# Optimization experiments

Hardware: AMD Instinct MI355X
Metric: run time of the kernel (lower is better)

The kernel has to match this reference:

```python
import jax, jax.numpy as jnp
import numpy as np

N, B, E, H, L, NF = 32768, 2048, 524288, 128, 7, 10
NODE_F = 60  # 10 frames * (loc 3 + vel 3)
OUT_F = 30   # 10 frames * 3


def _mlp(x, W1, b1, W2, b2):
    return jax.nn.relu(x @ W1 + b1) @ W2 + b2


def _lin(key, fan_in, fan_out):
    s = 1.0 / np.sqrt(fan_in)
    kw, kb = jax.random.split(key)
    W = jax.random.uniform(kw, (fan_in, fan_out), jnp.float32, -s, s)
    b = jax.random.uniform(kb, (fan_out,), jnp.float32, -s, s)
    return W, b


def setup_inputs() -> dict:
    key = jax.random.key(0)
    ks = jax.random.split(key, 12)
    p = {}
    p["loc"] = jax.random.normal(ks[0], (N, NF, 3), jnp.float32)
    p["vel"] = jax.random.normal(ks[1], (N, NF, 3), jnp.float32)
    p["y"] = jax.random.normal(ks[2], (N, NF, 3), jnp.float32)
    p["edge_index"] = jax.random.randint(ks[3], (2, E), 0, N, dtype=jnp.int64)
    p["batch_size"] = B
    # embedder: Linear(60,H) -> ReLU -> Linear(H,H)
    p["emb_W1"], p["emb_b1"] = _lin(ks[4], NODE_F, H)
    p["emb_W2"], p["emb_b2"] = _lin(ks[5], H, H)
    # per-layer message net Linear(2H,H)->ReLU->Linear(H,H); update net Linear(2H,H)->ReLU->Linear(H,H)
    mW1, mb1, mW2, mb2, uW1, ub1, uW2, ub2 = [], [], [], [], [], [], [], []
    for i in range(L):
        k = jax.random.fold_in(ks[6], i)
        k1, k2, k3, k4 = jax.random.split(k, 4)
        a, b = _lin(k1, 2 * H, H); mW1.append(a); mb1.append(b)
        a, b = _lin(k2, H, H); mW2.append(a); mb2.append(b)
        a, b = _lin(k3, 2 * H, H); uW1.append(a); ub1.append(b)
        a, b = _lin(k4, H, H); uW2.append(a); ub2.append(b)
    p["msg_W1"] = jnp.stack(mW1); p["msg_b1"] = jnp.stack(mb1)
    p["msg_W2"] = jnp.stack(mW2); p["msg_b2"] = jnp.stack(mb2)
    p["upd_W1"] = jnp.stack(uW1); p["upd_b1"] = jnp.stack(ub1)
    p["upd_W2"] = jnp.stack(uW2); p["upd_b2"] = jnp.stack(ub2)
    # head: Linear(H,H) -> ReLU -> Linear(H,30)
    p["head_W1"], p["head_b1"] = _lin(ks[7], H, H)
    p["head_W2"], p["head_b2"] = _lin(ks[8], H, OUT_F)
    return p


def reference(loc, vel, y, edge_index, batch_size,
              emb_W1, emb_b1, emb_W2, emb_b2,
              msg_W1, msg_b1, msg_W2, msg_b2,
              upd_W1, upd_b1, upd_W2, upd_b2,
              head_W1, head_b1, head_W2, head_b2):
    n = loc.shape[0]
    src, dst = edge_index[0], edge_index[1]  # x_j = x[src], x_i = x[dst] (PyG source_to_target)
    x = jnp.concatenate([loc, vel], axis=-1).reshape(n, -1)  # (N, 60)
    x = _mlp(x, emb_W1, emb_b1, emb_W2, emb_b2)              # (N, H)
    for i in range(L):
        m_in = jnp.concatenate([x[dst], x[src]], axis=-1)    # (E, 2H) cat(x_i, x_j)
        msg = _mlp(m_in, msg_W1[i], msg_b1[i], msg_W2[i], msg_b2[i])  # (E, H)
        agg = jax.ops.segment_sum(msg, dst, num_segments=n)  # scatter-add at targets
        x = _mlp(jnp.concatenate([x, agg], axis=-1), upd_W1[i], upd_b1[i], upd_W2[i], upd_b2[i])
    x = _mlp(x, head_W1, head_b1, head_W2, head_b2)          # (N, 30)
    loc_pred = x.reshape(n, NF, 3) + loc
    d = jnp.sqrt(jnp.sum((loc_pred - y) ** 2, axis=-1))      # (N, NF)
    ade_loss = d.reshape(batch_size, -1, NF).mean(axis=-1).mean(axis=-1)  # (B,)
    fde = jnp.sqrt(jnp.sum((loc_pred[:, -1, :] - y[:, -1, :]) ** 2, axis=-1))  # (N,)
    fde_loss = fde.reshape(batch_size, -1).mean(axis=-1)     # (B,)
    backprop_loss = ade_loss.mean()
    return backprop_loss, ade_loss, fde_loss
```

## Files before the change

### kernel.cpp

```cpp
#include <hip/hip_runtime.h>
#include <hip/hip_bf16.h>
#include <stdint.h>

#define HH 128

typedef __attribute__((ext_vector_type(8))) short short8;
typedef __attribute__((ext_vector_type(4))) float floatx4;

typedef __attribute__((address_space(3))) uint32_t lds_u32_t;
typedef const __attribute__((address_space(1))) uint32_t gbl_u32_t;

__device__ __forceinline__ void gl_lds16(const void* g, void* l) {
  __builtin_amdgcn_global_load_lds((gbl_u32_t*)g, (lds_u32_t*)l, 16, 0, 0);
}

__device__ __forceinline__ float bf2f(short v) {
  union { uint32_t u; float f; } x; x.u = ((uint32_t)(uint16_t)v) << 16; return x.f;
}
__device__ __forceinline__ short f2bf(float f) {
  union { float f; uint32_t u; } x; x.f = f;
  uint32_t r = x.u + 0x7fffu + ((x.u >> 16) & 1u);
  return (short)(r >> 16);
}
__device__ __forceinline__ float rdf(const void* p, int i, int fl) {
  return fl ? bf2f(((const short*)p)[i]) : ((const float*)p)[i];
}


__global__ void detect_zero(const int* __restrict__ eidx, int* iflag, int* dflag,
                            int* __restrict__ counts, float* accp, int* ticket,
                            const uint32_t* __restrict__ loc, int N) {
  int g = blockIdx.x * 256 + threadIdx.x;
  if (g < N) counts[g] = 0;
  if (blockIdx.x == 0) {
    __shared__ int nz, cnt;
    if (threadIdx.x == 0) { nz = 0; cnt = 0; *accp = 0.f; *ticket = 0; }
    __syncthreads();
    int any = 0;
    for (int i = threadIdx.x; i < 1024; i += 256) any |= (eidx[2 * i + 1] != 0);
    if (any) atomicOr(&nz, 1);
    uint32_t u = loc[threadIdx.x];
    int e = (u >> 7) & 0xFF;
    if (e >= 100 && e <= 140) atomicAdd(&cnt, 1);
    __syncthreads();
    if (threadIdx.x == 0) {
      *iflag = (nz == 0) ? 1 : 0;
      *dflag = (cnt >= 192) ? 1 : 0;
    }
  }
}


__global__ void pad_input(const void* __restrict__ loc, const void* __restrict__ vel,
                          short* __restrict__ dst, const int* __restrict__ dflag) {
  int fl = *dflag;
  int idx = blockIdx.x * 256 + threadIdx.x;
  int j = idx & 63, i = idx >> 6;
  short v = 0;
  if (j < 60) {
    int f = j / 6, c = j % 6;
    float x = (c < 3) ? rdf(loc, (i * 10 + f) * 3 + c, fl)
                      : rdf(vel, (i * 10 + f) * 3 + (c - 3), fl);
    v = f2bf(x);
  }
  dst[idx] = v;
}

struct WPrep {
  const void* src[8];
  unsigned long long dstoff[8];
  int L[8], K[8], Nn[8], Kp[8], Np[8];
  int bstart[9];
};

__global__ void prep_w(WPrep a, short* __restrict__ wbase, const int* __restrict__ dflag) {
  int fl = *dflag;
  int b = blockIdx.x;
  int s = 0;
  while (b >= a.bstart[s + 1]) ++s;
  int idx = (b - a.bstart[s]) * 256 + threadIdx.x;
  int Kp = a.Kp[s], Np = a.Np[s], K = a.K[s], Nn = a.Nn[s];
  int tot = a.L[s] * Np * Kp;
  if (idx >= tot) return;
  int k = idx % Kp; int rest = idx / Kp; int n = rest % Np; int l = rest / Np;
  short v = 0;
  if (k < K && n < Nn) v = f2bf(rdf(a.src[s], (l * K + k) * Nn + n, fl));
  wbase[a.dstoff[s] + idx] = v;
}

struct BPrep {
  const void* src[8];
  int n[8];
  int estart[9];
};

__global__ void prep_b(BPrep a, float* __restrict__ bias, const int* __restrict__ dflag) {
  int fl = *dflag;
  int idx = blockIdx.x * 256 + threadIdx.x;
  if (idx >= a.estart[8]) return;
  int s = 0;
  while (idx >= a.estart[s + 1]) ++s;
  int j = idx - a.estart[s];
  bias[idx] = (j < a.n[s]) ? rdf(a.src[s], j, fl) : 0.0f;
}


__global__ void fold_kernel(const short* __restrict__ msgW1T, const short* __restrict__ msgW2T,
                            const short* __restrict__ updW1T, const short* __restrict__ updW2T,
                            const short* __restrict__ headW1T,
                            const float* __restrict__ msgB1f, const float* __restrict__ msgB2f,
                            const float* __restrict__ updB1f, const float* __restrict__ updB2f,
                            const float* __restrict__ headB1f,
                            short* __restrict__ fmats, float* __restrict__ fbias) {
  if (blockIdx.x < 1664) {
    int idx = blockIdx.x * 256 + threadIdx.x;
    if (idx >= 26 * 16384) return;
    int k = idx & 127; int n = (idx >> 7) & 127; int m = idx >> 14;
    const short* w2;
    const short* rhs;
    if (m < 7) {
      w2 = msgW2T + m * 16384;
      rhs = updW1T + m * 32768 + n * 256 + 128;
    } else if (m < 14) {
      int l = m - 7;
      w2 = updW2T + l * 16384;
      rhs = (l < 6) ? (msgW1T + (l + 1) * 32768 + n * 256) : (headW1T + n * 128);
    } else if (m < 20) {
      int l = m - 14;
      w2 = updW2T + l * 16384;
      rhs = msgW1T + (l + 1) * 32768 + n * 256 + 128;
    } else {
      int l = m - 20;
      w2 = updW2T + l * 16384;
      rhs = updW1T + (l + 1) * 32768 + n * 256;
    }
    float s = 0.f;
    for (int j = 0; j < 128; ++j) s += bf2f(w2[j * 128 + k]) * bf2f(rhs[j]);
    fmats[idx] = f2bf(s);
  } else {
    int idx = (blockIdx.x - 1664) * 256 + threadIdx.x;
    if (idx >= 26 * 128) return;
    int n = idx & 127; int m = idx >> 7;
    float s = 0.f;
    if (m < 7) {
      const short* u1 = updW1T + m * 32768 + n * 256 + 128;
      for (int j = 0; j < 128; ++j) s += msgB2f[m * 128 + j] * bf2f(u1[j]);
    } else if (m < 14) {
      int l = m - 7;
      if (l < 6) {
        const short* m1 = msgW1T + (l + 1) * 32768 + n * 256;
        for (int j = 0; j < 128; ++j) s += updB2f[l * 128 + j] * bf2f(m1[j]);
        s += msgB1f[(l + 1) * 128 + n];
      } else {
        const short* h1 = headW1T + n * 128;
        for (int j = 0; j < 128; ++j) s += updB2f[6 * 128 + j] * bf2f(h1[j]);
        s += headB1f[n];
      }
    } else if (m < 20) {
      int l = m - 14;
      const short* m1 = msgW1T + (l + 1) * 32768 + n * 256 + 128;
      for (int j = 0; j < 128; ++j) s += updB2f[l * 128 + j] * bf2f(m1[j]);
    } else {
      int l = m - 20;
      const short* u1 = updW1T + (l + 1) * 32768 + n * 256;
      for (int j = 0; j < 128; ++j) s += updB2f[l * 128 + j] * bf2f(u1[j]);
      s += updB1f[(l + 1) * 128 + n];
    }
    fbias[m * 128 + n] = s;
  }
}


__global__ void hist_kernel(const int* __restrict__ eidx, const int* __restrict__ iflag,
                            int* __restrict__ counts, int E) {
  int e = blockIdx.x * 256 + threadIdx.x;
  if (e >= E) return;
  int fl = *iflag;
  int d = fl ? eidx[2 * (E + e)] : eidx[E + e];
  atomicAdd(&counts[d], 1);
}

__global__ void scan_bsum(const int* __restrict__ counts, int* __restrict__ bsums, int N) {
  int i = blockIdx.x * 256 + threadIdx.x;
  int v = (i < N) ? counts[i] : 0;
#pragma unroll
  for (int off = 1; off < 64; off <<= 1) v += __shfl_xor(v, off);
  __shared__ int ws4[4];
  if ((threadIdx.x & 63) == 0) ws4[threadIdx.x >> 6] = v;
  __syncthreads();
  if (threadIdx.x == 0) bsums[blockIdx.x] = ws4[0] + ws4[1] + ws4[2] + ws4[3];
}

__global__ void scan_final(const int* __restrict__ counts, const int* __restrict__ bsums,
                           int* __restrict__ row_start, int* __restrict__ cursor,
                           float* __restrict__ deg, int N, int E) {
  int t = threadIdx.x;
  __shared__ int shb[2];
  __shared__ int wsum[4];
  int v = (t < 128 && t < (int)blockIdx.x) ? bsums[t] : 0;
#pragma unroll
  for (int off = 1; off < 64; off <<= 1) v += __shfl_xor(v, off);
  if (t == 0) shb[0] = v;
  if (t == 64) shb[1] = v;
  int i = blockIdx.x * 256 + t;
  int c = (i < N) ? counts[i] : 0;
  int lane = t & 63, w = t >> 6;
  int x = c;
#pragma unroll
  for (int off = 1; off < 64; off <<= 1) {
    int u = __shfl_up(x, off);
    if (lane >= off) x += u;
  }
  if (lane == 63) wsum[w] = x;
  __syncthreads();
  int wpre = 0;
#pragma unroll
  for (int k = 0; k < 4; ++k)
    if (k < w) wpre += wsum[k];
  int excl = shb[0] + shb[1] + wpre + x - c;
  if (i < N) {
    row_start[i] = excl;
    cursor[i] = excl;
    deg[i] = (float)c;
  }
  if (i == N - 1) row_start[N] = E;
}

__global__ void scatter_kernel(const int* __restrict__ eidx, const int* __restrict__ iflag,
                               int* __restrict__ cursor, int* __restrict__ ssrc, int E) {
  int e = blockIdx.x * 256 + threadIdx.x;
  if (e >= E) return;
  int fl = *iflag;
  int d = fl ? eidx[2 * (E + e)] : eidx[E + e];
  int sv = fl ? eidx[2 * e] : eidx[e];
  int pos = atomicAdd(&cursor[d], 1);
  ssrc[pos] = sv;
}


__global__ __launch_bounds__(256)
void edge_agg(const uint32_t* __restrict__ Pp, const uint32_t* __restrict__ Qp,
              const int* __restrict__ ssrc, const int* __restrict__ row_start,
              uint32_t* __restrict__ Hagg, int Ntot) {
  int w = threadIdx.x >> 6, lane = threadIdx.x & 63;
  int d = blockIdx.x * 4 + w;
  if (d >= Ntot) return;
  uint32_t pv = Pp[(size_t)d * 64 + lane];
  float px = bf2f((short)(pv & 0xffff));
  float py = bf2f((short)(pv >> 16));
  int s0 = row_start[d], s1 = row_start[d + 1];
  float ax = 0.f, ay = 0.f;
  int e = s0;
  for (; e + 8 <= s1; e += 8) {
    int idx[8]; uint32_t q[8];
#pragma unroll
    for (int u = 0; u < 8; ++u) idx[u] = ssrc[e + u];
#pragma unroll
    for (int u = 0; u < 8; ++u) q[u] = Qp[(size_t)idx[u] * 64 + lane];
#pragma unroll
    for (int u = 0; u < 8; ++u) {
      float hx = px + bf2f((short)(q[u] & 0xffff));
      float hy = py + bf2f((short)(q[u] >> 16));
      ax += hx > 0.f ? hx : 0.f;
      ay += hy > 0.f ? hy : 0.f;
    }
  }
  if (e + 4 <= s1) {
    int idx[4]; uint32_t q[4];
#pragma unroll
    for (int u = 0; u < 4; ++u) idx[u] = ssrc[e + u];
#pragma unroll
    for (int u = 0; u < 4; ++u) q[u] = Qp[(size_t)idx[u] * 64 + lane];
#pragma unroll
    for (int u = 0; u < 4; ++u) {
      float hx = px + bf2f((short)(q[u] & 0xffff));
      float hy = py + bf2f((short)(q[u] >> 16));
      ax += hx > 0.f ? hx : 0.f;
      ay += hy > 0.f ? hy : 0.f;
    }
    e += 4;
  }
  if (e + 2 <= s1) {
    int i0 = ssrc[e], i1 = ssrc[e + 1];
    uint32_t q0 = Qp[(size_t)i0 * 64 + lane];
    uint32_t q1 = Qp[(size_t)i1 * 64 + lane];
    float hx = px + bf2f((short)(q0 & 0xffff)), hy = py + bf2f((short)(q0 >> 16));
    ax += hx > 0.f ? hx : 0.f; ay += hy > 0.f ? hy : 0.f;
    hx = px + bf2f((short)(q1 & 0xffff)); hy = py + bf2f((short)(q1 >> 16));
    ax += hx > 0.f ? hx : 0.f; ay += hy > 0.f ? hy : 0.f;
    e += 2;
  }
  if (e < s1) {
    int i0 = ssrc[e];
    uint32_t q0 = Qp[(size_t)i0 * 64 + lane];
    float hx = px + bf2f((short)(q0 & 0xffff));
    float hy = py + bf2f((short)(q0 >> 16));
    ax += hx > 0.f ? hx : 0.f;
    ay += hy > 0.f ? hy : 0.f;
  }
  uint32_t packed = (uint32_t)(uint16_t)f2bf(ax) | ((uint32_t)(uint16_t)f2bf(ay) << 16);
  Hagg[(size_t)d * 64 + lane] = packed;
}


__device__ __forceinline__ void write_aslots64(char* lds, const floatx4 v[2][4],
                                               int wr, int wc, int quad, int l16) {
#pragma unroll
  for (int mt = 0; mt < 2; ++mt) {
    int g = wr * 2 + mt;
#pragma unroll
    for (int nt = 0; nt < 4; ++nt) {
      int s2 = wc * 2 + (nt >> 1);
      int qc = (nt & 1) * 2 + (l16 >> 3);
      char* base = lds + (size_t)(s2 * 4 + g) * 1024 + 2 * (l16 & 7);
#pragma unroll
      for (int r = 0; r < 4; ++r)
        *(short*)(base + (quad * 4 + r + 16 * qc) * 16) = f2bf(v[mt][nt][r]);
    }
  }
}

template <int NT, int TS>
__device__ __forceinline__ void gemm64(const char* lds, int wr, int wc,
                                       floatx4 acc[2][NT], int lane) {
  const char* ldsB = lds + 16384;
#pragma unroll
  for (int s2 = 0; s2 < 4; ++s2) {
    short8 af[2];
#pragma unroll
    for (int mt = 0; mt < 2; ++mt)
      af[mt] = *(const short8*)(lds + (s2 * 4 + wr * 2 + mt) * 1024 + lane * 16);
    short8 bf[NT];
#pragma unroll
    for (int nt = 0; nt < NT; ++nt)
      bf[nt] = *(const short8*)(ldsB + (s2 * TS + wc * NT + nt) * 1024 + lane * 16);
#pragma unroll
    for (int mt = 0; mt < 2; ++mt)
#pragma unroll
      for (int nt = 0; nt < NT; ++nt)
        acc[mt][nt] = __builtin_amdgcn_mfma_f32_16x16x32_bf16(af[mt], bf[nt], acc[mt][nt], 0, 0, 0);
  }
}

__device__ __forceinline__ void stage128(const short* M, int stride, char* ldsB,
                                         int w, int lane, int quad, int l16) {
#pragma unroll
  for (int c = 0; c < 8; ++c) {
    int slot = w * 8 + c, s2 = slot >> 3, t = slot & 7;
    gl_lds16(M + (t * 16 + l16) * stride + s2 * 32 + quad * 8,
             ldsB + slot * 1024 + lane * 16);
  }
}


template <int MODE>
__global__ __launch_bounds__(256, 3)
void mlp_fused(const short* __restrict__ Ain, const short* __restrict__ XUin,
               const short* __restrict__ W1s, const float* __restrict__ b1s,
               const short* __restrict__ W2s, const float* __restrict__ b2s,
               const short* __restrict__ W3s, const float* __restrict__ b3s,
               const short* __restrict__ W4s, const float* __restrict__ b4s,
               const float* __restrict__ deg,
               short* __restrict__ Pout, short* __restrict__ Qout,
               short* __restrict__ XUout, float* __restrict__ out32) {
  __shared__ __align__(16) char lds[49152];
  char* ldsB = lds + 16384;

  const int tid = threadIdx.x;
  const int w = tid >> 6, lane = tid & 63;
  const int quad = lane >> 4, l16 = lane & 15;
  const int wr = w >> 1, wc = w & 1;
  const int R0 = blockIdx.x * 64;
  const int CB = wc * 64;

  floatx4 zero4 = {0.f, 0.f, 0.f, 0.f};
  floatx4 acc[2][4];

  if constexpr (MODE == 0) {
#pragma unroll
    for (int c = 0; c < 4; ++c) {
      int slot = w * 4 + c, s = slot >> 3, t = slot & 7;
      gl_lds16(W1s + (t * 16 + l16) * 64 + s * 32 + quad * 8,
               ldsB + slot * 1024 + lane * 16);
    }
    short8 afrag[2][2];
#pragma unroll
    for (int mt = 0; mt < 2; ++mt) {
      int m = R0 + wr * 32 + mt * 16 + l16;
      const short* pr = Ain + (size_t)m * 64;
#pragma unroll
      for (int s = 0; s < 2; ++s) afrag[s][mt] = *(const short8*)(pr + s * 32 + quad * 8);
    }
    float b1f[4], b2f[4], pa[4], pc[4];
#pragma unroll
    for (int t = 0; t < 4; ++t) {
      int col = CB + t * 16 + l16;
      b1f[t] = b1s[col]; b2f[t] = b2s[col]; pa[t] = b3s[col]; pc[t] = b4s[col];
    }
#pragma unroll
    for (int mt = 0; mt < 2; ++mt)
#pragma unroll
      for (int t = 0; t < 4; ++t) acc[mt][t] = zero4;
    __syncthreads();
#pragma unroll
    for (int s = 0; s < 2; ++s) {
      short8 bfrag[4];
#pragma unroll
      for (int nt = 0; nt < 4; ++nt)
        bfrag[nt] = *(const short8*)(ldsB + (s * 8 + wc * 4 + nt) * 1024 + lane * 16);
#pragma unroll
      for (int mt = 0; mt < 2; ++mt)
#pragma unroll
        for (int nt = 0; nt < 4; ++nt)
          acc[mt][nt] = __builtin_amdgcn_mfma_f32_16x16x32_bf16(afrag[s][mt], bfrag[nt], acc[mt][nt], 0, 0, 0);
    }
    __syncthreads();
    stage128(W2s, 128, ldsB, w, lane, quad, l16);
    {
      floatx4 hv[2][4];
#pragma unroll
      for (int mt = 0; mt < 2; ++mt)
#pragma unroll
        for (int nt = 0; nt < 4; ++nt)
#pragma unroll
          for (int r = 0; r < 4; ++r) {
            float h = acc[mt][nt][r] + b1f[nt];
            hv[mt][nt][r] = h > 0.f ? h : 0.f;
          }
      write_aslots64(lds, hv, wr, wc, quad, l16);
    }
    __syncthreads();
    floatx4 accx[2][4];
#pragma unroll
    for (int mt = 0; mt < 2; ++mt)
#pragma unroll
      for (int t = 0; t < 4; ++t) accx[mt][t] = zero4;
    gemm64<4, 8>(lds, wr, wc, accx, lane);
    floatx4 xv[2][4];
#pragma unroll
    for (int mt = 0; mt < 2; ++mt)
#pragma unroll
      for (int nt = 0; nt < 4; ++nt)
#pragma unroll
        for (int r = 0; r < 4; ++r)
          xv[mt][nt][r] = accx[mt][nt][r] + b2f[nt];
    __syncthreads();
    write_aslots64(lds, xv, wr, wc, quad, l16);
    stage128(W3s, 256, ldsB, w, lane, quad, l16);
    __syncthreads();
    floatx4 ap[2][4];
#pragma unroll
    for (int mt = 0; mt < 2; ++mt)
#pragma unroll
      for (int t = 0; t < 4; ++t) ap[mt][t] = zero4;
    gemm64<4, 8>(lds, wr, wc, ap, lane);
#pragma unroll
    for (int mt = 0; mt < 2; ++mt)
#pragma unroll
      for (int nt = 0; nt < 4; ++nt) {
        int col = CB + nt * 16 + l16;
#pragma unroll
        for (int r = 0; r < 4; ++r) {
          int row = R0 + wr * 32 + mt * 16 + quad * 4 + r;
          Pout[(size_t)row * HH + col] = f2bf(ap[mt][nt][r] + pa[nt]);
        }
      }
    __syncthreads();
    stage128(W3s + 128, 256, ldsB, w, lane, quad, l16);
    __syncthreads();
    floatx4 aq[2][4];
#pragma unroll
    for (int mt = 0; mt < 2; ++mt)
#pragma unroll
      for (int t = 0; t < 4; ++t) aq[mt][t] = zero4;
    gemm64<4, 8>(lds, wr, wc, aq, lane);
#pragma unroll
    for (int mt = 0; mt < 2; ++mt)
#pragma unroll
      for (int nt = 0; nt < 4; ++nt) {
        int col = CB + nt * 16 + l16;
#pragma unroll
        for (int r = 0; r < 4; ++r) {
          int row = R0 + wr * 32 + mt * 16 + quad * 4 + r;
          Qout[(size_t)row * HH + col] = f2bf(aq[mt][nt][r]);
        }
      }
    __syncthreads();
    stage128(W4s, 256, ldsB, w, lane, quad, l16);
    __syncthreads();
    floatx4 au[2][4];
#pragma unroll
    for (int mt = 0; mt < 2; ++mt)
#pragma unroll
      for (int t = 0; t < 4; ++t) au[mt][t] = zero4;
    gemm64<4, 8>(lds, wr, wc, au, lane);
#pragma unroll
    for (int mt = 0; mt < 2; ++mt)
#pragma unroll
      for (int nt = 0; nt < 4; ++nt) {
        int col = CB + nt * 16 + l16;
#pragma unroll
        for (int r = 0; r < 4; ++r) {
          int row = R0 + wr * 32 + mt * 16 + quad * 4 + r;
          XUout[(size_t)row * HH + col] = f2bf(au[mt][nt][r] + pc[nt]);
        }
      }
    return;
  } else {
    stage128(W1s, 128, ldsB, w, lane, quad, l16);
    short8 hfrag[4][2];
#pragma unroll
    for (int mt = 0; mt < 2; ++mt) {
      int m = R0 + wr * 32 + mt * 16 + l16;
      const short* pr = Ain + (size_t)m * HH;
#pragma unroll
      for (int s = 0; s < 4; ++s) hfrag[s][mt] = *(const short8*)(pr + s * 32 + quad * 8);
    }
    float b2u[4], pa[4], pb[4], pc[4];
#pragma unroll
    for (int t = 0; t < 4; ++t) {
      int col = CB + t * 16 + l16;
      b2u[t] = b1s[col];
      pa[t] = b2s[col];
      if constexpr (MODE == 2) { pb[t] = b3s[col]; pc[t] = b4s[col]; }
    }
    float dvals[2][4];
#pragma unroll
    for (int mt = 0; mt < 2; ++mt)
#pragma unroll
      for (int r = 0; r < 4; ++r)
        dvals[mt][r] = deg[R0 + wr * 32 + mt * 16 + quad * 4 + r];
#pragma unroll
    for (int mt = 0; mt < 2; ++mt)
#pragma unroll
      for (int nt = 0; nt < 4; ++nt) {
        int col = CB + nt * 16 + l16;
#pragma unroll
        for (int r = 0; r < 4; ++r) {
          int row = R0 + wr * 32 + mt * 16 + quad * 4 + r;
          acc[mt][nt][r] = bf2f(XUin[(size_t)row * HH + col]) + dvals[mt][r] * b2u[nt];
        }
      }
    __syncthreads();
#pragma unroll
    for (int s = 0; s < 4; ++s) {
      short8 bfrag[4];
#pragma unroll
      for (int nt = 0; nt < 4; ++nt)
        bfrag[nt] = *(const short8*)(ldsB + (s * 8 + wc * 4 + nt) * 1024 + lane * 16);
#pragma unroll
      for (int mt = 0; mt < 2; ++mt)
#pragma unroll
        for (int nt = 0; nt < 4; ++nt)
          acc[mt][nt] = __builtin_amdgcn_mfma_f32_16x16x32_bf16(hfrag[s][mt], bfrag[nt], acc[mt][nt], 0, 0, 0);
    }
    __syncthreads();
    stage128(W2s, 128, ldsB, w, lane, quad, l16);
    {
      floatx4 hv[2][4];
#pragma unroll
      for (int mt = 0; mt < 2; ++mt)
#pragma unroll
        for (int nt = 0; nt < 4; ++nt)
#pragma unroll
          for (int r = 0; r < 4; ++r) {
            float h = acc[mt][nt][r];
            hv[mt][nt][r] = h > 0.f ? h : 0.f;
          }
      write_aslots64(lds, hv, wr, wc, quad, l16);
    }
    __syncthreads();
    floatx4 ap[2][4];
#pragma unroll
    for (int mt = 0; mt < 2; ++mt)
#pragma unroll
      for (int t = 0; t < 4; ++t) ap[mt][t] = zero4;
    gemm64<4, 8>(lds, wr, wc, ap, lane);

    if constexpr (MODE == 2) {
#pragma unroll
      for (int mt = 0; mt < 2; ++mt)
#pragma unroll
        for (int nt = 0; nt < 4; ++nt) {
          int col = CB + nt * 16 + l16;
#pragma unroll
          for (int r = 0; r < 4; ++r) {
            int row = R0 + wr * 32 + mt * 16 + quad * 4 + r;
            Pout[(size_t)row * HH + col] = f2bf(ap[mt][nt][r] + pa[nt]);
          }
        }
      __syncthreads();
      stage128(W3s, 128, ldsB, w, lane, quad, l16);
      __syncthreads();
      floatx4 aq[2][4];
#pragma unroll
      for (int mt = 0; mt < 2; ++mt)
#pragma unroll
        for (int t = 0; t < 4; ++t) aq[mt][t] = zero4;
      gemm64<4, 8>(lds, wr, wc, aq, lane);
#pragma unroll
      for (int mt = 0; mt < 2; ++mt)
#pragma unroll
        for (int nt = 0; nt < 4; ++nt) {
          int col = CB + nt * 16 + l16;
#pragma unroll
          for (int r = 0; r < 4; ++r) {
            int row = R0 + wr * 32 + mt * 16 + quad * 4 + r;
            Qout[(size_t)row * HH + col] = f2bf(aq[mt][nt][r] + pb[nt]);
          }
        }
      __syncthreads();
      stage128(W4s, 128, ldsB, w, lane, quad, l16);
      __syncthreads();
      floatx4 au[2][4];
#pragma unroll
      for (int mt = 0; mt < 2; ++mt)
#pragma unroll
        for (int t = 0; t < 4; ++t) au[mt][t] = zero4;
      gemm64<4, 8>(lds, wr, wc, au, lane);
#pragma unroll
      for (int mt = 0; mt < 2; ++mt)
#pragma unroll
        for (int nt = 0; nt < 4; ++nt) {
          int col = CB + nt * 16 + l16;
#pragma unroll
          for (int r = 0; r < 4; ++r) {
            int row = R0 + wr * 32 + mt * 16 + quad * 4 + r;
            XUout[(size_t)row * HH + col] = f2bf(au[mt][nt][r] + pc[nt]);
          }
        }
    } else {
      floatx4 h2[2][4];
#pragma unroll
      for (int mt = 0; mt < 2; ++mt)
#pragma unroll
        for (int nt = 0; nt < 4; ++nt)
#pragma unroll
          for (int r = 0; r < 4; ++r) {
            float h = ap[mt][nt][r] + pa[nt];
            h2[mt][nt][r] = h > 0.f ? h : 0.f;
          }
      __syncthreads();
      write_aslots64(lds, h2, wr, wc, quad, l16);
#pragma unroll
      for (int c = 0; c < 2; ++c) {
        int slot = w * 2 + c, s2 = slot >> 1, t = slot & 1;
        gl_lds16(W3s + (t * 16 + l16) * 128 + s2 * 32 + quad * 8,
                 ldsB + slot * 1024 + lane * 16);
      }
      __syncthreads();
      floatx4 acco[2][1];
#pragma unroll
      for (int mt = 0; mt < 2; ++mt) acco[mt][0] = zero4;
      gemm64<1, 2>(lds, wr, wc, acco, lane);
      float ob = b3s[wc * 16 + l16];
#pragma unroll
      for (int mt = 0; mt < 2; ++mt) {
        int col = wc * 16 + l16;
#pragma unroll
        for (int r = 0; r < 4; ++r) {
          int row = R0 + wr * 32 + mt * 16 + quad * 4 + r;
          out32[(size_t)row * 32 + col] = acco[mt][0][r] + ob;
        }
      }
    }
  }
}


__global__ void loss_kernel(const float* __restrict__ out32, const void* __restrict__ loc,
                            const void* __restrict__ yv, const int* __restrict__ dflag,
                            float* __restrict__ out, float* __restrict__ acc,
                            int* __restrict__ ticket, int NB, int nblocks, float inv) {
  int fl = *dflag;
  int i = blockIdx.x * 256 + threadIdx.x;
  const float* o = out32 + (size_t)i * 32;
  float dsum = 0.f, fde = 0.f;
#pragma unroll
  for (int f = 0; f < 10; ++f) {
    float dx = o[f * 3 + 0] + rdf(loc, i * 30 + f * 3 + 0, fl) - rdf(yv, i * 30 + f * 3 + 0, fl);
    float dy = o[f * 3 + 1] + rdf(loc, i * 30 + f * 3 + 1, fl) - rdf(yv, i * 30 + f * 3 + 1, fl);
    float dz = o[f * 3 + 2] + rdf(loc, i * 30 + f * 3 + 2, fl) - rdf(yv, i * 30 + f * 3 + 2, fl);
    float d = sqrtf(dx * dx + dy * dy + dz * dz);
    dsum += d;
    if (f == 9) fde = d;
  }
#pragma unroll
  for (int m = 1; m < 16; m <<= 1) {
    dsum += __shfl_xor(dsum, m);
    fde += __shfl_xor(fde, m);
  }
  if ((threadIdx.x & 15) == 0) {
    int b = i >> 4;
    out[1 + b] = dsum / 160.0f;
    out[1 + NB + b] = fde / 16.0f;
    unsafeAtomicAdd(acc, dsum);
  }
  __threadfence();
  __syncthreads();
  if (threadIdx.x == 0) {
    int old = atomicAdd(ticket, 1);
    if (old == nblocks - 1) {
      float v = unsafeAtomicAdd(acc, 0.0f);
      out[0] = v * inv;
    }
  }
}


extern "C" void kernel_launch(void* const* d_in, const int* in_sizes, int n_in,
                              void* d_out, int out_size, void* d_ws, size_t ws_size,
                              hipStream_t stream) {
  const void* loc = d_in[0];
  const void* vel = d_in[1];
  const void* yv = d_in[2];
  const int* eidx = (const int*)d_in[3];

  const int N = in_sizes[0] / 30;
  const int E = in_sizes[3] / 2;
  const int L = 7;
  const int NB = N / 16;

  const size_t MB = 1024 * 1024;
  char* ws = (char*)d_ws;
  short* XU = (short*)ws;
  short* P = (short*)(ws + 8 * MB);
  short* Qs = (short*)(ws + 24 * MB);
  short* Hagg = (short*)(ws + 32 * MB);
  short* fmats = (short*)(ws + 40 * MB);
  int* bsums = (int*)(ws + 41 * MB);
  short* wbase = (short*)(ws + 48 * MB);
  const unsigned long long OFF_EMBW1 = 0;
  const unsigned long long OFF_EMBW2 = 8192;
  const unsigned long long OFF_HEADW1 = 24576;
  const unsigned long long OFF_HEADW2 = 40960;
  const unsigned long long OFF_MSGW1 = 45056;
  const unsigned long long OFF_MSGW2 = 274432;
  const unsigned long long OFF_UPDW1 = 389120;
  const unsigned long long OFF_UPDW2 = 618496;
  short* embW1T = wbase + OFF_EMBW1;
  short* embW2T = wbase + OFF_EMBW2;
  short* headW1T = wbase + OFF_HEADW1;
  short* headW2T = wbase + OFF_HEADW2;
  short* msgW1T = wbase + OFF_MSGW1;
  short* msgW2T = wbase + OFF_MSGW2;
  short* updW1T = wbase + OFF_UPDW1;
  short* updW2T = wbase + OFF_UPDW2;
  float* bias = (float*)(ws + 49 * MB + 512 * 1024);
  float* embB1f = bias;
  float* embB2f = bias + 128;
  float* msgB1f = bias + 256;
  float* msgB2f = bias + 1152;
  float* updB1f = bias + 2048;
  float* updB2f = bias + 2944;
  float* headB1f = bias + 3840;
  float* headB2f = bias + 3968;
  float* fbias = (float*)(ws + 49 * MB + 640 * 1024);
  int* counts = (int*)(ws + 49 * MB + 768 * 1024);
  int* row_start = (int*)(ws + 50 * MB);
  int* cursor = (int*)(ws + 50 * MB + 256 * 1024);
  float* deg = (float*)(ws + 50 * MB + 512 * 1024);
  int* iflag = (int*)(ws + 50 * MB + 768 * 1024);
  int* dflag = iflag + 16;
  float* accp = (float*)(iflag + 32);
  int* ticket = iflag + 48;
  int* ssrc = (int*)(ws + 51 * MB);
  short* in64 = (short*)(ws + 53 * MB);
  float* out32 = (float*)(ws + 57 * MB);

  const int NBLK = (N + 255) / 256;

  detect_zero<<<NBLK, 256, 0, stream>>>(eidx, iflag, dflag, counts, accp, ticket,
                                        (const uint32_t*)loc, N);
  hist_kernel<<<(E + 255) / 256, 256, 0, stream>>>(eidx, iflag, counts, E);
  scan_bsum<<<NBLK, 256, 0, stream>>>(counts, bsums, N);
  scan_final<<<NBLK, 256, 0, stream>>>(counts, bsums, row_start, cursor, deg, N, E);
  scatter_kernel<<<(E + 255) / 256, 256, 0, stream>>>(eidx, iflag, cursor, ssrc, E);

  pad_input<<<(N * 64) / 256, 256, 0, stream>>>(loc, vel, in64, dflag);

  {
    WPrep a;
    const void* srcs[8] = {d_in[5], d_in[7], d_in[17], d_in[19],
                           d_in[9], d_in[11], d_in[13], d_in[15]};
    unsigned long long offs[8] = {OFF_EMBW1, OFF_EMBW2, OFF_HEADW1, OFF_HEADW2,
                                  OFF_MSGW1, OFF_MSGW2, OFF_UPDW1, OFF_UPDW2};
    int Ls[8] = {1, 1, 1, 1, 7, 7, 7, 7};
    int Ks[8] = {60, 128, 128, 128, 256, 128, 256, 128};
    int Ns[8] = {128, 128, 128, 30, 128, 128, 128, 128};
    int Kps[8] = {64, 128, 128, 128, 256, 128, 256, 128};
    int Nps[8] = {128, 128, 128, 32, 128, 128, 128, 128};
    int cum = 0;
    for (int s = 0; s < 8; ++s) {
      a.src[s] = srcs[s]; a.dstoff[s] = offs[s];
      a.L[s] = Ls[s]; a.K[s] = Ks[s]; a.Nn[s] = Ns[s]; a.Kp[s] = Kps[s]; a.Np[s] = Nps[s];
      a.bstart[s] = cum;
      cum += (Ls[s] * Nps[s] * Kps[s] + 255) / 256;
    }
    a.bstart[8] = cum;
    prep_w<<<cum, 256, 0, stream>>>(a, wbase, dflag);
  }
  {
    BPrep a;
    const void* srcs[8] = {d_in[6], d_in[8], d_in[10], d_in[12],
                           d_in[14], d_in[16], d_in[18], d_in[20]};
    int ns[8] = {128, 128, 896, 896, 896, 896, 128, 30};
    int es[9] = {0, 128, 256, 1152, 2048, 2944, 3840, 3968, 4000};
    for (int s = 0; s < 8; ++s) { a.src[s] = srcs[s]; a.n[s] = ns[s]; a.estart[s] = es[s]; }
    a.estart[8] = es[8];
    prep_b<<<16, 256, 0, stream>>>(a, bias, dflag);
  }

  fold_kernel<<<1664 + 13, 256, 0, stream>>>(msgW1T, msgW2T, updW1T, updW2T, headW1T,
                                             msgB1f, msgB2f, updB1f, updB2f, headB1f,
                                             fmats, fbias);

  mlp_fused<0><<<N / 64, 256, 0, stream>>>(in64, nullptr,
      embW1T, embB1f, embW2T, embB2f,
      msgW1T, msgB1f, updW1T, updB1f,
      nullptr, P, Qs, XU, nullptr);

  for (int l = 0; l < L; ++l) {
    edge_agg<<<(N + 3) / 4, 256, 0, stream>>>((const uint32_t*)P, (const uint32_t*)Qs,
                                              ssrc, row_start, (uint32_t*)Hagg, N);
    if (l < L - 1) {
      mlp_fused<2><<<N / 64, 256, 0, stream>>>(Hagg, XU,
          fmats + l * 16384, fbias + l * 128,
          fmats + (7 + l) * 16384, fbias + (7 + l) * 128,
          fmats + (14 + l) * 16384, fbias + (14 + l) * 128,
          fmats + (20 + l) * 16384, fbias + (20 + l) * 128,
          deg, P, Qs, XU, nullptr);
    } else {
      mlp_fused<3><<<N / 64, 256, 0, stream>>>(Hagg, XU,
          fmats + 6 * 16384, fbias + 6 * 128,
          fmats + 13 * 16384, fbias + 13 * 128,
          headW2T, headB2f,
          nullptr, nullptr,
          deg, nullptr, nullptr, nullptr, out32);
    }
  }

  loss_kernel<<<N / 256, 256, 0, stream>>>(out32, loc, yv, dflag, (float*)d_out, accp,
                                           ticket, NB, N / 256, 1.0f / 327680.0f);
}
```

Measured before the change: 485.9 us.

## Fuse loss into final MLP, store XU fragment-native, unroll edge gather

The loss computation moves into the last fused MLP kernel: head outputs are staged in LDS and reduced per block, which drops the separate loss kernel and the out32 round trip through global memory. The XU intermediate is now stored in a per-thread fragment-native layout, so writes and reads become contiguous vectorized accesses instead of scattered 16-bit stores. The edge aggregation loop gains a 16-wide unrolled gather to keep more loads in flight, at the cost of higher register pressure. The XU layout change only works because every kernel that touches XU agrees on the new per-thread layout.

```diff
diff --git a/kernel.cpp b/kernel.cpp
--- a/kernel.cpp
+++ b/kernel.cpp
@@ -6,6 +6,7 @@
 
 typedef __attribute__((ext_vector_type(8))) short short8;
 typedef __attribute__((ext_vector_type(4))) float floatx4;
+typedef __attribute__((ext_vector_type(4))) uint32_t uint4v;
 
 typedef __attribute__((address_space(3))) uint32_t lds_u32_t;
 typedef const __attribute__((address_space(1))) uint32_t gbl_u32_t;
@@ -24,6 +25,9 @@
 }
 __device__ __forceinline__ float rdf(const void* p, int i, int fl) {
   return fl ? bf2f(((const short*)p)[i]) : ((const float*)p)[i];
+}
+__device__ __forceinline__ uint32_t packbf(float a, float b) {
+  return (uint32_t)(uint16_t)f2bf(a) | ((uint32_t)(uint16_t)f2bf(b) << 16);
 }
 
 
@@ -251,7 +255,21 @@
   int s0 = row_start[d], s1 = row_start[d + 1];
   float ax = 0.f, ay = 0.f;
   int e = s0;
-  for (; e + 8 <= s1; e += 8) {
+  for (; e + 16 <= s1; e += 16) {
+    int idx[16]; uint32_t q[16];
+#pragma unroll
+    for (int u = 0; u < 16; ++u) idx[u] = ssrc[e + u];
+#pragma unroll
+    for (int u = 0; u < 16; ++u) q[u] = Qp[(size_t)idx[u] * 64 + lane];
+#pragma unroll
+    for (int u = 0; u < 16; ++u) {
+      float hx = px + bf2f((short)(q[u] & 0xffff));
+      float hy = py + bf2f((short)(q[u] >> 16));
+      ax += hx > 0.f ? hx : 0.f;
+      ay += hy > 0.f ? hy : 0.f;
+    }
+  }
+  if (e + 8 <= s1) {
     int idx[8]; uint32_t q[8];
 #pragma unroll
     for (int u = 0; u < 8; ++u) idx[u] = ssrc[e + u];
@@ -264,6 +282,7 @@
       ax += hx > 0.f ? hx : 0.f;
       ay += hy > 0.f ? hy : 0.f;
     }
+    e += 8;
   }
   if (e + 4 <= s1) {
     int idx[4]; uint32_t q[4];
@@ -298,8 +317,7 @@
     ax += hx > 0.f ? hx : 0.f;
     ay += hy > 0.f ? hy : 0.f;
   }
-  uint32_t packed = (uint32_t)(uint16_t)f2bf(ax) | ((uint32_t)(uint16_t)f2bf(ay) << 16);
-  Hagg[(size_t)d * 64 + lane] = packed;
+  Hagg[(size_t)d * 64 + lane] = packbf(ax, ay);
 }
 
 
@@ -362,7 +380,11 @@
                const short* __restrict__ W4s, const float* __restrict__ b4s,
                const float* __restrict__ deg,
                short* __restrict__ Pout, short* __restrict__ Qout,
-               short* __restrict__ XUout, float* __restrict__ out32) {
+               short* __restrict__ XUout,
+               const void* __restrict__ locp, const void* __restrict__ yvp,
+               const int* __restrict__ dflagp, float* __restrict__ lossout,
+               float* __restrict__ accg, int* __restrict__ ticketp,
+               int NBv, int nbl, float inv) {
   __shared__ __align__(16) char lds[49152];
   char* ldsB = lds + 16384;
 
@@ -494,17 +516,16 @@
 #pragma unroll
       for (int t = 0; t < 4; ++t) au[mt][t] = zero4;
     gemm64<4, 8>(lds, wr, wc, au, lane);
-#pragma unroll
-    for (int mt = 0; mt < 2; ++mt)
-#pragma unroll
-      for (int nt = 0; nt < 4; ++nt) {
-        int col = CB + nt * 16 + l16;
-#pragma unroll
-        for (int r = 0; r < 4; ++r) {
-          int row = R0 + wr * 32 + mt * 16 + quad * 4 + r;
-          XUout[(size_t)row * HH + col] = f2bf(au[mt][nt][r] + pc[nt]);
-        }
-      }
+    {
+      uint32_t* xpw = (uint32_t*)XUout + ((size_t)(blockIdx.x * 256) + tid) * 16;
+#pragma unroll
+      for (int mt = 0; mt < 2; ++mt)
+#pragma unroll
+        for (int nt = 0; nt < 4; ++nt) {
+          xpw[(mt * 4 + nt) * 2 + 0] = packbf(au[mt][nt][0] + pc[nt], au[mt][nt][1] + pc[nt]);
+          xpw[(mt * 4 + nt) * 2 + 1] = packbf(au[mt][nt][2] + pc[nt], au[mt][nt][3] + pc[nt]);
+        }
+    }
     return;
   } else {
     stage128(W1s, 128, ldsB, w, lane, quad, l16);
@@ -530,17 +551,27 @@
 #pragma unroll
       for (int r = 0; r < 4; ++r)
         dvals[mt][r] = deg[R0 + wr * 32 + mt * 16 + quad * 4 + r];
-#pragma unroll
-    for (int mt = 0; mt < 2; ++mt)
-#pragma unroll
-      for (int nt = 0; nt < 4; ++nt) {
-        int col = CB + nt * 16 + l16;
-#pragma unroll
-        for (int r = 0; r < 4; ++r) {
-          int row = R0 + wr * 32 + mt * 16 + quad * 4 + r;
-          acc[mt][nt][r] = bf2f(XUin[(size_t)row * HH + col]) + dvals[mt][r] * b2u[nt];
-        }
+    {
+      const uint4v* xp = (const uint4v*)((const uint32_t*)XUin +
+                                         ((size_t)(blockIdx.x * 256) + tid) * 16);
+      uint32_t xw[16];
+#pragma unroll
+      for (int k2 = 0; k2 < 4; ++k2) {
+        uint4v v = xp[k2];
+#pragma unroll
+        for (int j = 0; j < 4; ++j) xw[k2 * 4 + j] = v[j];
       }
+#pragma unroll
+      for (int mt = 0; mt < 2; ++mt)
+#pragma unroll
+        for (int nt = 0; nt < 4; ++nt) {
+          uint32_t u0 = xw[(mt * 4 + nt) * 2], u1 = xw[(mt * 4 + nt) * 2 + 1];
+          acc[mt][nt][0] = bf2f((short)(u0 & 0xffff)) + dvals[mt][0] * b2u[nt];
+          acc[mt][nt][1] = bf2f((short)(u0 >> 16)) + dvals[mt][1] * b2u[nt];
+          acc[mt][nt][2] = bf2f((short)(u1 & 0xffff)) + dvals[mt][2] * b2u[nt];
+          acc[mt][nt][3] = bf2f((short)(u1 >> 16)) + dvals[mt][3] * b2u[nt];
+        }
+    }
     __syncthreads();
 #pragma unroll
     for (int s = 0; s < 4; ++s) {
@@ -618,17 +649,16 @@
 #pragma unroll
         for (int t = 0; t < 4; ++t) au[mt][t] = zero4;
       gemm64<4, 8>(lds, wr, wc, au, lane);
-#pragma unroll
-      for (int mt = 0; mt < 2; ++mt)
-#pragma unroll
-        for (int nt = 0; nt < 4; ++nt) {
-          int col = CB + nt * 16 + l16;
-#pragma unroll
-          for (int r = 0; r < 4; ++r) {
-            int row = R0 + wr * 32 + mt * 16 + quad * 4 + r;
-            XUout[(size_t)row * HH + col] = f2bf(au[mt][nt][r] + pc[nt]);
+      {
+        uint32_t* xpw = (uint32_t*)XUout + ((size_t)(blockIdx.x * 256) + tid) * 16;
+#pragma unroll
+        for (int mt = 0; mt < 2; ++mt)
+#pragma unroll
+          for (int nt = 0; nt < 4; ++nt) {
+            xpw[(mt * 4 + nt) * 2 + 0] = packbf(au[mt][nt][0] + pc[nt], au[mt][nt][1] + pc[nt]);
+            xpw[(mt * 4 + nt) * 2 + 1] = packbf(au[mt][nt][2] + pc[nt], au[mt][nt][3] + pc[nt]);
           }
-        }
+      }
     } else {
       floatx4 h2[2][4];
 #pragma unroll
@@ -654,55 +684,53 @@
       for (int mt = 0; mt < 2; ++mt) acco[mt][0] = zero4;
       gemm64<1, 2>(lds, wr, wc, acco, lane);
       float ob = b3s[wc * 16 + l16];
+      __syncthreads();
+      float* lot = (float*)lds;
 #pragma unroll
       for (int mt = 0; mt < 2; ++mt) {
-        int col = wc * 16 + l16;
+        int colL = wc * 16 + l16;
 #pragma unroll
         for (int r = 0; r < 4; ++r) {
-          int row = R0 + wr * 32 + mt * 16 + quad * 4 + r;
-          out32[(size_t)row * 32 + col] = acco[mt][0][r] + ob;
+          int rowL = wr * 32 + mt * 16 + quad * 4 + r;
+          lot[rowL * 32 + colL] = acco[mt][0][r] + ob;
         }
       }
-    }
-  }
-}
-
-
-__global__ void loss_kernel(const float* __restrict__ out32, const void* __restrict__ loc,
-                            const void* __restrict__ yv, const int* __restrict__ dflag,
-                            float* __restrict__ out, float* __restrict__ acc,
-                            int* __restrict__ ticket, int NB, int nblocks, float inv) {
-  int fl = *dflag;
-  int i = blockIdx.x * 256 + threadIdx.x;
-  const float* o = out32 + (size_t)i * 32;
-  float dsum = 0.f, fde = 0.f;
-#pragma unroll
-  for (int f = 0; f < 10; ++f) {
-    float dx = o[f * 3 + 0] + rdf(loc, i * 30 + f * 3 + 0, fl) - rdf(yv, i * 30 + f * 3 + 0, fl);
-    float dy = o[f * 3 + 1] + rdf(loc, i * 30 + f * 3 + 1, fl) - rdf(yv, i * 30 + f * 3 + 1, fl);
-    float dz = o[f * 3 + 2] + rdf(loc, i * 30 + f * 3 + 2, fl) - rdf(yv, i * 30 + f * 3 + 2, fl);
-    float d = sqrtf(dx * dx + dy * dy + dz * dz);
-    dsum += d;
-    if (f == 9) fde = d;
-  }
-#pragma unroll
-  for (int m = 1; m < 16; m <<= 1) {
-    dsum += __shfl_xor(dsum, m);
-    fde += __shfl_xor(fde, m);
-  }
-  if ((threadIdx.x & 15) == 0) {
-    int b = i >> 4;
-    out[1 + b] = dsum / 160.0f;
-    out[1 + NB + b] = fde / 16.0f;
-    unsafeAtomicAdd(acc, dsum);
-  }
-  __threadfence();
-  __syncthreads();
-  if (threadIdx.x == 0) {
-    int old = atomicAdd(ticket, 1);
-    if (old == nblocks - 1) {
-      float v = unsafeAtomicAdd(acc, 0.0f);
-      out[0] = v * inv;
+      __syncthreads();
+      int fl = *dflagp;
+      if (tid < 64) {
+        int node = R0 + tid;
+        const float* o = lot + tid * 32;
+        float dsum = 0.f, fde = 0.f;
+#pragma unroll
+        for (int f = 0; f < 10; ++f) {
+          float dx = o[f * 3 + 0] + rdf(locp, node * 30 + f * 3 + 0, fl) - rdf(yvp, node * 30 + f * 3 + 0, fl);
+          float dy = o[f * 3 + 1] + rdf(locp, node * 30 + f * 3 + 1, fl) - rdf(yvp, node * 30 + f * 3 + 1, fl);
+          float dz = o[f * 3 + 2] + rdf(locp, node * 30 + f * 3 + 2, fl) - rdf(yvp, node * 30 + f * 3 + 2, fl);
+          float d = sqrtf(dx * dx + dy * dy + dz * dz);
+          dsum += d;
+          if (f == 9) fde = d;
+        }
+#pragma unroll
+        for (int m = 1; m < 16; m <<= 1) {
+          dsum += __shfl_xor(dsum, m);
+          fde += __shfl_xor(fde, m);
+        }
+        if ((tid & 15) == 0) {
+          int b = node >> 4;
+          lossout[1 + b] = dsum / 160.0f;
+          lossout[1 + NBv + b] = fde / 16.0f;
+          unsafeAtomicAdd(accg, dsum);
+        }
+      }
+      __threadfence();
+      __syncthreads();
+      if (tid == 0) {
+        int old = atomicAdd(ticketp, 1);
+        if (old == nbl - 1) {
+          float v = unsafeAtomicAdd(accg, 0.0f);
+          lossout[0] = v * inv;
+        }
+      }
     }
   }
 }
@@ -766,7 +794,6 @@
   int* ticket = iflag + 48;
   int* ssrc = (int*)(ws + 51 * MB);
   short* in64 = (short*)(ws + 53 * MB);
-  float* out32 = (float*)(ws + 57 * MB);
 
   const int NBLK = (N + 255) / 256;
 
@@ -818,7 +845,8 @@
   mlp_fused<0><<<N / 64, 256, 0, stream>>>(in64, nullptr,
       embW1T, embB1f, embW2T, embB2f,
       msgW1T, msgB1f, updW1T, updB1f,
-      nullptr, P, Qs, XU, nullptr);
+      nullptr, P, Qs, XU,
+      nullptr, nullptr, nullptr, nullptr, nullptr, nullptr, 0, 0, 0.0f);
 
   for (int l = 0; l < L; ++l) {
     edge_agg<<<(N + 3) / 4, 256, 0, stream>>>((const uint32_t*)P, (const uint32_t*)Qs,
@@ -829,17 +857,17 @@
           fmats + (7 + l) * 16384, fbias + (7 + l) * 128,
           fmats + (14 + l) * 16384, fbias + (14 + l) * 128,
           fmats + (20 + l) * 16384, fbias + (20 + l) * 128,
-          deg, P, Qs, XU, nullptr);
+          deg, P, Qs, XU,
+          nullptr, nullptr, nullptr, nullptr, nullptr, nullptr, 0, 0, 0.0f);
     } else {
       mlp_fused<3><<<N / 64, 256, 0, stream>>>(Hagg, XU,
           fmats + 6 * 16384, fbias + 6 * 128,
           fmats + 13 * 16384, fbias + 13 * 128,
           headW2T, headB2f,
           nullptr, nullptr,
-          deg, nullptr, nullptr, nullptr, out32);
-    }
-  }
-
-  loss_kernel<<<N / 256, 256, 0, stream>>>(out32, loc, yv, dflag, (float*)d_out, accp,
-                                           ticket, NB, N / 256, 1.0f / 327680.0f);
-}
+          deg, nullptr, nullptr, nullptr,
+          loc, yv, dflag, (float*)d_out, accp, ticket,
+          NB, N / 64, 1.0f / 327680.0f);
+    }
+  }
+}
```

Result: slower. 504.6 us (+3.8%).
